# Performance work log

Measured on AMD Instinct MI355X. Metric: run time of the kernel, lower is better.

The kernel has to match this reference:

```python
import jax, jax.numpy as jnp
import numpy as np

B, N, M = 4, 2048, 2048
DIM, DIM_KEYS, DIM_OUT = 512, 512, 512
HEADS, DIM_HEAD = 8, 64
INNER = HEADS * DIM_HEAD


def setup_inputs() -> dict:
    key = jax.random.key(0)
    ks = jax.random.split(key, 8)
    x = jax.random.normal(ks[0], (B, N, DIM), dtype=jnp.float32)
    context = jax.random.normal(ks[1], (B, M, DIM_KEYS), dtype=jnp.float32)
    Wq = jax.random.normal(ks[2], (DIM, INNER), dtype=jnp.float32) / np.sqrt(DIM)
    Wkv = jax.random.normal(ks[3], (DIM_KEYS, 2 * INNER), dtype=jnp.float32) / np.sqrt(DIM_KEYS)
    null_k = jax.random.normal(ks[4], (DIM_HEAD,), dtype=jnp.float32)
    null_v = jax.random.normal(ks[5], (DIM_HEAD,), dtype=jnp.float32)
    Wout = jax.random.normal(ks[6], (INNER, DIM_OUT), dtype=jnp.float32) / np.sqrt(INNER)
    bout = jnp.zeros((DIM_OUT,), dtype=jnp.float32)
    return {"x": x, "context": context, "Wq": Wq, "Wkv": Wkv,
            "null_k": null_k, "null_v": null_v, "Wout": Wout, "bout": bout}


def reference(x, context, Wq, Wkv, null_k, null_v, Wout, bout):
    b = x.shape[0]
    scale = DIM_HEAD ** (-0.5)
    q = x @ Wq                      # [b, n, inner]
    kv = context @ Wkv              # [b, m, 2*inner]
    k, v = jnp.split(kv, 2, axis=-1)
    # [b, h, n, d]
    q = q.reshape(b, -1, HEADS, DIM_HEAD).transpose(0, 2, 1, 3)
    k = k.reshape(b, -1, HEADS, DIM_HEAD).transpose(0, 2, 1, 3)
    v = v.reshape(b, -1, HEADS, DIM_HEAD).transpose(0, 2, 1, 3)
    # prepend null key/value token: [b, h, 1, d]
    nk = jnp.broadcast_to(null_k, (b, HEADS, 1, DIM_HEAD))
    nv = jnp.broadcast_to(null_v, (b, HEADS, 1, DIM_HEAD))
    k = jnp.concatenate((nk, k), axis=-2)  # [b, h, m+1, d]
    v = jnp.concatenate((nv, v), axis=-2)
    q = jnp.tanh(q)
    k = jnp.tanh(k)
    sim = jnp.einsum('bhid,bhjd->bhij', q, k) * scale  # [b, h, n, m+1]
    attn = jax.nn.softmax(sim, axis=-1)
    out = jnp.einsum('bhij,bhjd->bhid', attn, v)       # [b, h, n, d]
    out = out.transpose(0, 2, 1, 3).reshape(b, -1, INNER)  # [b, n, inner]
    return out @ Wout + bout
```

## Files before the change

### kernel.cpp

```cpp
#include <hip/hip_runtime.h>
#include <hip/hip_bf16.h>
#include <stdint.h>

#define B_    4
#define N_    2048
#define M_    2048
#define DIMX  512
#define INNER 512
#define H_    8
#define DH    64
#define MK    2049
#define MKP   2112

#define QSCALE  0.18033688011f
#define SM_BIAS -11.5415605f

using u16 = unsigned short;
using u32 = unsigned int;

typedef __attribute__((ext_vector_type(8))) short short8;
typedef __attribute__((ext_vector_type(4))) float f32x4;

#if defined(__has_builtin)
# if __has_builtin(__builtin_amdgcn_exp2f)
#  define EXP2(x) __builtin_amdgcn_exp2f(x)
# endif
#endif
#ifndef EXP2
# define EXP2(x) exp2f(x)
#endif

__device__ __forceinline__ u16 bfc(float f){
  __hip_bfloat16 h = __float2bfloat16(f);
  return *reinterpret_cast<u16*>(&h);
}
__device__ __forceinline__ u32 bfpk(float lo, float hi){
  return (u32)bfc(lo) | ((u32)bfc(hi) << 16);
}

__global__ __launch_bounds__(256) void transpose_all(
    const float* __restrict__ Wq, const float* __restrict__ Wkv,
    const float* __restrict__ Wout,
    u16* __restrict__ Wqt, u16* __restrict__ Wkvt, u16* __restrict__ Woutt)
{
  const int z = blockIdx.z;
  const float* in = (z == 0) ? Wq : (z == 1) ? Wkv : Wout;
  u16* out        = (z == 0) ? Wqt : (z == 1) ? Wkvt : Woutt;
  const int C     = (z == 1) ? 1024 : 512;
  const int R     = 512;
  if (blockIdx.x * 64 >= C) return;

  __shared__ float tl[64][65];
  const int t = threadIdx.x;
  const int c0 = blockIdx.x * 64, r0 = blockIdx.y * 64;
  const int col = t & 63, rb = t >> 6;
  #pragma unroll
  for (int j = 0; j < 16; ++j){
    const int row = rb + j*4;
    tl[row][col] = in[(size_t)(r0 + row) * C + c0 + col];
  }
  __syncthreads();
  #pragma unroll
  for (int j = 0; j < 16; ++j){
    const int orow = rb + j*4;
    out[(size_t)(c0 + orow) * R + r0 + col] = bfc(tl[col][orow]);
  }
}

__global__ __launch_bounds__(256, 3) void fused_proj(
    const float* __restrict__ x, const float* __restrict__ ctx,
    const u16* __restrict__ Wqt, const u16* __restrict__ Wkvt,
    u16* __restrict__ qb, u16* __restrict__ kb, u16* __restrict__ vb)
{
  __shared__ __align__(16) short At[2][128*32];
  __shared__ __align__(16) short Bl[2][128*32];

  const int flat = blockIdx.x;
  const int tile = (flat & 7) * 96 + (flat >> 3);
  const bool isq = tile < 256;
  const int lt   = isq ? tile : tile - 256;
  const int gx   = isq ? 4 : 8;
  const int row0 = (lt / gx) * 128, col0 = (lt % gx) * 128;
  const float* A = isq ? x : ctx;
  const u16*  Bt = isq ? Wqt : Wkvt;

  const int tid = threadIdx.x;
  const int w = tid >> 6, lane = tid & 63;
  const int c = lane & 15, g = lane >> 4;
  const int wr = (w >> 1) * 64, wc = (w & 1) * 64;

  f32x4 acc[4][4] = {};

  const int srow = tid >> 1, sj = (tid & 1) * 2;
  const int swz0 = ((sj  ) ^ ((srow >> 1) & 3)) << 4;
  const int swz1 = ((sj+1) ^ ((srow >> 1) & 3)) << 4;

  float4 a0, a1, a2, a3;
  uint4  b0, b1;
  const float* asrc = A  + (size_t)(row0 + srow) * DIMX + sj*8;
  const u16*   bsrc = Bt + (size_t)(col0 + srow) * DIMX + sj*8;

  a0 = ((const float4*)asrc)[0]; a1 = ((const float4*)asrc)[1];
  a2 = ((const float4*)asrc)[2]; a3 = ((const float4*)asrc)[3];
  b0 = ((const uint4*)bsrc)[0];  b1 = ((const uint4*)bsrc)[1];
  {
    uint4 t0, t1;
    t0.x = bfpk(a0.x, a0.y); t0.y = bfpk(a0.z, a0.w);
    t0.z = bfpk(a1.x, a1.y); t0.w = bfpk(a1.z, a1.w);
    t1.x = bfpk(a2.x, a2.y); t1.y = bfpk(a2.z, a2.w);
    t1.z = bfpk(a3.x, a3.y); t1.w = bfpk(a3.z, a3.w);
    *(uint4*)((char*)At[0] + srow*64 + swz0) = t0;
    *(uint4*)((char*)At[0] + srow*64 + swz1) = t1;
    *(uint4*)((char*)Bl[0] + srow*64 + swz0) = b0;
    *(uint4*)((char*)Bl[0] + srow*64 + swz1) = b1;
  }

  int cur = 0;
  #pragma unroll 4
  for (int kk = 0; kk < 16; ++kk){
    __syncthreads();
    if (kk < 15){
      const float* an = asrc + (kk+1)*32;
      const u16*   bn = bsrc + (kk+1)*32;
      a0 = ((const float4*)an)[0]; a1 = ((const float4*)an)[1];
      a2 = ((const float4*)an)[2]; a3 = ((const float4*)an)[3];
      b0 = ((const uint4*)bn)[0];  b1 = ((const uint4*)bn)[1];
    }

    short8 af[4], bf[4];
    #pragma unroll
    for (int m = 0; m < 4; ++m){
      const int row = wr + m*16 + c;
      af[m] = *(const short8*)((char*)At[cur] + row*64 + ((g ^ ((row>>1)&3)) << 4));
    }
    #pragma unroll
    for (int n = 0; n < 4; ++n){
      const int row = wc + n*16 + c;
      bf[n] = *(const short8*)((char*)Bl[cur] + row*64 + ((g ^ ((row>>1)&3)) << 4));
    }
    __builtin_amdgcn_s_setprio(1);
    #pragma unroll
    for (int m = 0; m < 4; ++m)
      #pragma unroll
      for (int n = 0; n < 4; ++n)
        acc[m][n] = __builtin_amdgcn_mfma_f32_16x16x32_bf16(af[m], bf[n], acc[m][n], 0, 0, 0);
    __builtin_amdgcn_s_setprio(0);

    if (kk < 15){
      uint4 t0, t1;
      t0.x = bfpk(a0.x, a0.y); t0.y = bfpk(a0.z, a0.w);
      t0.z = bfpk(a1.x, a1.y); t0.w = bfpk(a1.z, a1.w);
      t1.x = bfpk(a2.x, a2.y); t1.y = bfpk(a2.z, a2.w);
      t1.z = bfpk(a3.x, a3.y); t1.w = bfpk(a3.z, a3.w);
      char* An = (char*)At[cur ^ 1];
      char* Bn = (char*)Bl[cur ^ 1];
      *(uint4*)(An + srow*64 + swz0) = t0;
      *(uint4*)(An + srow*64 + swz1) = t1;
      *(uint4*)(Bn + srow*64 + swz0) = b0;
      *(uint4*)(Bn + srow*64 + swz1) = b1;
      cur ^= 1;
    }
  }

  #pragma unroll
  for (int m = 0; m < 4; ++m){
    #pragma unroll
    for (int n = 0; n < 4; ++n){
      #pragma unroll
      for (int rr = 0; rr < 4; ++rr){
        const int R = row0 + wr + m*16 + g*4 + rr;
        const int col = col0 + wc + n*16 + c;
        const float v = acc[m][n][rr];
        if (isq){
          qb[(size_t)R * INNER + col] = bfc(tanhf(v) * QSCALE);
        } else {
          const int bidx = R >> 11, mm = R & 2047;
          if (col < INNER){
            const int h = col >> 6, d = col & 63;
            kb[((size_t)(bidx*H_ + h) * MKP + (mm + 1)) * DH + d] = bfc(tanhf(v));
          } else {
            const int cc = col - INNER;
            const int h = cc >> 6, d = cc & 63;
            vb[((size_t)(bidx*H_ + h) * MKP + (mm + 1)) * DH + d] = bfc(v);
          }
        }
      }
    }
  }
}

__global__ __launch_bounds__(256) void mgemm_out(
    const u16* __restrict__ A, const u16* __restrict__ Bt,
    float* __restrict__ Cf, const float* __restrict__ bias)
{
  __shared__ __align__(16) short At[2][128*32];
  __shared__ __align__(16) short Bl[2][128*32];

  const int flat = blockIdx.x;
  const int tile = (flat & 7) * 32 + (flat >> 3);
  const int row0 = (tile >> 2) * 128, col0 = (tile & 3) * 128;

  const int tid = threadIdx.x;
  const int w = tid >> 6, lane = tid & 63;
  const int c = lane & 15, g = lane >> 4;
  const int wr = (w >> 1) * 64, wc = (w & 1) * 64;

  f32x4 acc[4][4] = {};

  const int srow = tid >> 1, sj = (tid & 1) * 2;
  const int swz0 = ((sj  ) ^ ((srow >> 1) & 3)) << 4;
  const int swz1 = ((sj+1) ^ ((srow >> 1) & 3)) << 4;

  uint4 ta0, ta1, b0, b1;
  const u16* asrc = A  + (size_t)(row0 + srow) * INNER + sj*8;
  const u16* bsrc = Bt + (size_t)(col0 + srow) * INNER + sj*8;

  ta0 = ((const uint4*)asrc)[0]; ta1 = ((const uint4*)asrc)[1];
  b0  = ((const uint4*)bsrc)[0]; b1  = ((const uint4*)bsrc)[1];
  *(uint4*)((char*)At[0] + srow*64 + swz0) = ta0;
  *(uint4*)((char*)At[0] + srow*64 + swz1) = ta1;
  *(uint4*)((char*)Bl[0] + srow*64 + swz0) = b0;
  *(uint4*)((char*)Bl[0] + srow*64 + swz1) = b1;

  int cur = 0;
  #pragma unroll 4
  for (int kk = 0; kk < 16; ++kk){
    __syncthreads();
    if (kk < 15){
      const u16* an = asrc + (kk+1)*32;
      const u16* bn = bsrc + (kk+1)*32;
      ta0 = ((const uint4*)an)[0]; ta1 = ((const uint4*)an)[1];
      b0  = ((const uint4*)bn)[0]; b1  = ((const uint4*)bn)[1];
    }

    short8 af[4], bf[4];
    #pragma unroll
    for (int m = 0; m < 4; ++m){
      const int row = wr + m*16 + c;
      af[m] = *(const short8*)((char*)At[cur] + row*64 + ((g ^ ((row>>1)&3)) << 4));
    }
    #pragma unroll
    for (int n = 0; n < 4; ++n){
      const int row = wc + n*16 + c;
      bf[n] = *(const short8*)((char*)Bl[cur] + row*64 + ((g ^ ((row>>1)&3)) << 4));
    }
    __builtin_amdgcn_s_setprio(1);
    #pragma unroll
    for (int m = 0; m < 4; ++m)
      #pragma unroll
      for (int n = 0; n < 4; ++n)
        acc[m][n] = __builtin_amdgcn_mfma_f32_16x16x32_bf16(af[m], bf[n], acc[m][n], 0, 0, 0);
    __builtin_amdgcn_s_setprio(0);

    if (kk < 15){
      char* An = (char*)At[cur ^ 1];
      char* Bn = (char*)Bl[cur ^ 1];
      *(uint4*)(An + srow*64 + swz0) = ta0;
      *(uint4*)(An + srow*64 + swz1) = ta1;
      *(uint4*)(Bn + srow*64 + swz0) = b0;
      *(uint4*)(Bn + srow*64 + swz1) = b1;
      cur ^= 1;
    }
  }

  #pragma unroll
  for (int m = 0; m < 4; ++m){
    #pragma unroll
    for (int n = 0; n < 4; ++n){
      #pragma unroll
      for (int rr = 0; rr < 4; ++rr){
        const int R = row0 + wr + m*16 + g*4 + rr;
        const int col = col0 + wc + n*16 + c;
        Cf[(size_t)R * 512 + col] = acc[m][n][rr] + bias[col];
      }
    }
  }
}

__global__ __launch_bounds__(256) void vtrans(
    const u16* __restrict__ vb, u16* __restrict__ vt,
    const float* __restrict__ nk, const float* __restrict__ nv,
    u16* __restrict__ kb)
{
  __shared__ short tl[64][72];
  const int t = threadIdx.x;
  const int mt = blockIdx.x, bh = blockIdx.y;
  {
    const int mr = t >> 2, chb = (t & 3) * 2;
    const u16* src = vb + ((size_t)bh * MKP + mt*64 + mr) * DH + chb*8;
    uint4 a = ((const uint4*)src)[0];
    uint4 b = ((const uint4*)src)[1];
    *(uint4*)((char*)tl + mr*144 + chb*16)     = a;
    *(uint4*)((char*)tl + mr*144 + (chb+1)*16) = b;
  }
  __syncthreads();
  {
    const int d = t >> 2, chb = (t & 3) * 2;
    #pragma unroll
    for (int j = 0; j < 2; ++j){
      const int mbase = (chb + j) * 8;
      u16 s[8];
      #pragma unroll
      for (int e = 0; e < 8; ++e) s[e] = (u16)tl[mbase + e][d];
      if (mt == 0 && mbase == 0) s[0] = bfc(nv[d]);
      uint4 o;
      o.x = (u32)s[0] | ((u32)s[1] << 16);
      o.y = (u32)s[2] | ((u32)s[3] << 16);
      o.z = (u32)s[4] | ((u32)s[5] << 16);
      o.w = (u32)s[6] | ((u32)s[7] << 16);
      *(uint4*)(vt + ((size_t)bh * DH + d) * MKP + mt*64 + mbase) = o;
    }
    if (mt == 0 && (t & 3) == 0)
      kb[(size_t)bh * MKP * DH + d] = bfc(tanhf(nk[d]));
  }
}

__global__ __launch_bounds__(256) void attn_mfma(
    const u16* __restrict__ qb, const u16* __restrict__ kb,
    const u16* __restrict__ vt, u16* __restrict__ aob)
{
  __shared__ __align__(16) short Kl[2][64*64];
  __shared__ __align__(16) short Vl[2][64*64];
  __shared__ __align__(16) short Pl[4][16*64];

  const int tid  = threadIdx.x;
  const int w    = tid >> 6;
  const int lane = tid & 63;
  const int c    = lane & 15;
  const int g    = lane >> 4;
  const int bh   = blockIdx.y, b = bh >> 3, h = bh & 7;
  const int qbase = blockIdx.x * 64 + w * 16;
  const int xr   = (c & 7) << 4;

  short8 qf0, qf1;
  {
    const u16* qrow = qb + ((size_t)(b*N_) + qbase + c) * INNER + h * DH;
    qf0 = *(const short8*)(qrow + g*8);
    qf1 = *(const short8*)(qrow + 32 + g*8);
  }

  f32x4 o[4] = {};
  float l_c = 0.f;

  const u16* kbase = kb + (size_t)bh * MKP * DH;
  const u16* vbase = vt + (size_t)bh * DH * MKP;
  const int srow = tid >> 2, sch = (tid & 3) * 2;
  const int swz0 = ((sch  ) ^ (srow & 7)) << 4;
  const int swz1 = ((sch+1) ^ (srow & 7)) << 4;

  uint4 rk0, rk1, rv0, rv1;
  {
    const u16* ksrc = kbase + (size_t)srow * DH + sch*8;
    rk0 = ((const uint4*)ksrc)[0]; rk1 = ((const uint4*)ksrc)[1];
    const u16* vsrc = vbase + (size_t)srow * MKP + sch*8;
    rv0 = ((const uint4*)vsrc)[0]; rv1 = ((const uint4*)vsrc)[1];
  }
  *(uint4*)((char*)Kl[0] + srow*128 + swz0) = rk0;
  *(uint4*)((char*)Kl[0] + srow*128 + swz1) = rk1;
  *(uint4*)((char*)Vl[0] + srow*128 + swz0) = rv0;
  *(uint4*)((char*)Vl[0] + srow*128 + swz1) = rv1;

  int cur = 0;
  for (int kt = 0; kt < 33; ++kt){
    __syncthreads();
    if (kt < 32){
      const u16* ksrc = kbase + (size_t)((kt+1)*64 + srow) * DH + sch*8;
      rk0 = ((const uint4*)ksrc)[0]; rk1 = ((const uint4*)ksrc)[1];
      const u16* vsrc = vbase + (size_t)srow * MKP + (kt+1)*64 + sch*8;
      rv0 = ((const uint4*)vsrc)[0]; rv1 = ((const uint4*)vsrc)[1];
    }

    const char* Kc = (const char*)Kl[cur];
    const char* Vc = (const char*)Vl[cur];
    char*       Pw = (char*)Pl + w*2048;

    f32x4 sv[4];
    __builtin_amdgcn_s_setprio(1);
    #pragma unroll
    for (int s = 0; s < 4; ++s){
      f32x4 a = {SM_BIAS, SM_BIAS, SM_BIAS, SM_BIAS};
      #pragma unroll
      for (int hh = 0; hh < 2; ++hh){
        short8 kf = *(const short8*)(Kc + (s*16 + c)*128 + ((hh*64 + g*16) ^ xr));
        a = __builtin_amdgcn_mfma_f32_16x16x32_bf16(kf, hh ? qf1 : qf0, a, 0, 0, 0);
      }
      sv[s] = a;
    }
    __builtin_amdgcn_s_setprio(0);

    if (kt == 32){
      #pragma unroll
      for (int s = 0; s < 4; ++s)
        #pragma unroll
        for (int r = 0; r < 4; ++r)
          if (s | r) sv[s][r] = -1e30f;
      if (g) sv[0][0] = -1e30f;
    }

    float psum = 0.f;
    #pragma unroll
    for (int s = 0; s < 4; ++s){
      const float p0 = EXP2(sv[s][0]);
      const float p1 = EXP2(sv[s][1]);
      const float p2 = EXP2(sv[s][2]);
      const float p3 = EXP2(sv[s][3]);
      psum += (p0 + p1) + (p2 + p3);
      uint2 pk;
      pk.x = bfpk(p0, p1);
      pk.y = bfpk(p2, p3);
      *(uint2*)(Pw + c*128 + ((((2*s + (g>>1)) ^ (c&7)) << 4) | ((g&1)*8))) = pk;
    }
    psum += __shfl_xor(psum, 16);
    psum += __shfl_xor(psum, 32);
    l_c += psum;

    __builtin_amdgcn_s_setprio(1);
    #pragma unroll
    for (int hh = 0; hh < 2; ++hh){
      short8 pf = *(const short8*)(Pw + c*128 + (((hh*4 + g) ^ (c&7)) << 4));
      #pragma unroll
      for (int D = 0; D < 4; ++D){
        short8 vf = *(const short8*)(Vc + (D*16 + c)*128 + ((hh*64 + g*16) ^ xr));
        o[D] = __builtin_amdgcn_mfma_f32_16x16x32_bf16(pf, vf, o[D], 0, 0, 0);
      }
    }
    __builtin_amdgcn_s_setprio(0);

    if (kt < 32){
      char* Kn = (char*)Kl[cur ^ 1];
      char* Vn = (char*)Vl[cur ^ 1];
      *(uint4*)(Kn + srow*128 + swz0) = rk0;
      *(uint4*)(Kn + srow*128 + swz1) = rk1;
      *(uint4*)(Vn + srow*128 + swz0) = rv0;
      *(uint4*)(Vn + srow*128 + swz1) = rv1;
      cur ^= 1;
    }
  }

  const float inv = 1.f / l_c;
  #pragma unroll
  for (int r = 0; r < 4; ++r){
    const float ir = __shfl(inv, g*4 + r, 16);
    const size_t nrow = (size_t)(b*N_) + qbase + g*4 + r;
    #pragma unroll
    for (int D = 0; D < 4; ++D)
      aob[nrow * INNER + h*DH + D*16 + c] = bfc(o[D][r] * ir);
  }
}

extern "C" void kernel_launch(void* const* d_in, const int* in_sizes, int n_in,
                              void* d_out, int out_size, void* d_ws, size_t ws_size,
                              hipStream_t stream)
{
  const float* x    = (const float*)d_in[0];
  const float* ctx  = (const float*)d_in[1];
  const float* Wq   = (const float*)d_in[2];
  const float* Wkv  = (const float*)d_in[3];
  const float* nk   = (const float*)d_in[4];
  const float* nv   = (const float*)d_in[5];
  const float* Wout = (const float*)d_in[6];
  const float* bout = (const float*)d_in[7];
  float* out = (float*)d_out;

  char* ws = (char*)d_ws;
  u16* qb    = (u16*)(ws);
  u16* kbB   = (u16*)(ws +  8388608);
  u16* vbB   = (u16*)(ws + 17039360);
  u16* vtb   = (u16*)(ws + 25690112);
  u16* Wqt   = (u16*)(ws + 34340864);
  u16* Wkvt  = (u16*)(ws + 34865152);
  u16* Woutt = (u16*)(ws + 35913728);
  u16* aoB   = vbB;

  transpose_all<<<dim3(16, 8, 3), 256, 0, stream>>>(Wq, Wkv, Wout, Wqt, Wkvt, Woutt);

  fused_proj<<<768, 256, 0, stream>>>(x, ctx, Wqt, Wkvt, qb, kbB, vbB);
  vtrans<<<dim3(33, 32), 256, 0, stream>>>(vbB, vtb, nk, nv, kbB);
  attn_mfma<<<dim3(32, 32), 256, 0, stream>>>(qb, kbB, vtb, aoB);
  mgemm_out<<<256, 256, 0, stream>>>(aoB, Woutt, out, bout);
}
```

Baseline: 121.9 us.

## Pre-convert inputs to bf16, deepen GEMM prefetch, remap attention grid

Adds a separate kernel that converts x and context to bf16 ahead of time, so the projection GEMM loads bf16 directly instead of converting fp32 inside its main loop. Both GEMMs now keep two k-tiles of global loads in flight, using a manually unrolled double-register prefetch. mgemm_out gets an occupancy hint in its launch bounds. The attention launch becomes a 1D grid with the block index remapped so that head/batch pairs are spread across XCDs. The cost is an extra kernel launch and an extra fp32 read and bf16 write/read of the activations.

```diff
diff --git a/kernel.cpp b/kernel.cpp
--- a/kernel.cpp
+++ b/kernel.cpp
@@ -38,6 +38,21 @@
   return (u32)bfc(lo) | ((u32)bfc(hi) << 16);
 }
 
+__global__ __launch_bounds__(256) void convert_bf(
+    const float* __restrict__ x, const float* __restrict__ ctx,
+    u16* __restrict__ xb, u16* __restrict__ cb)
+{
+  const float* in = blockIdx.z ? ctx : x;
+  u16* out        = blockIdx.z ? cb : xb;
+  const int i = blockIdx.x * 256 + threadIdx.x;
+  float4 a = ((const float4*)in)[i*2];
+  float4 b = ((const float4*)in)[i*2+1];
+  uint4 t;
+  t.x = bfpk(a.x, a.y); t.y = bfpk(a.z, a.w);
+  t.z = bfpk(b.x, b.y); t.w = bfpk(b.z, b.w);
+  ((uint4*)out)[i] = t;
+}
+
 __global__ __launch_bounds__(256) void transpose_all(
     const float* __restrict__ Wq, const float* __restrict__ Wkv,
     const float* __restrict__ Wout,
@@ -67,8 +82,30 @@
   }
 }
 
+#define PROJ_COMPUTE(bi)                                                      \
+  {                                                                           \
+    short8 af[4], bf[4];                                                      \
+    _Pragma("unroll")                                                         \
+    for (int m = 0; m < 4; ++m){                                              \
+      const int row = wr + m*16 + c;                                          \
+      af[m] = *(const short8*)((char*)At[bi] + row*64 + ((g ^ ((row>>1)&3)) << 4)); \
+    }                                                                         \
+    _Pragma("unroll")                                                         \
+    for (int n = 0; n < 4; ++n){                                              \
+      const int row = wc + n*16 + c;                                          \
+      bf[n] = *(const short8*)((char*)Bl[bi] + row*64 + ((g ^ ((row>>1)&3)) << 4)); \
+    }                                                                         \
+    __builtin_amdgcn_s_setprio(1);                                            \
+    _Pragma("unroll")                                                         \
+    for (int m = 0; m < 4; ++m)                                               \
+      _Pragma("unroll")                                                       \
+      for (int n = 0; n < 4; ++n)                                             \
+        acc[m][n] = __builtin_amdgcn_mfma_f32_16x16x32_bf16(af[m], bf[n], acc[m][n], 0, 0, 0); \
+    __builtin_amdgcn_s_setprio(0);                                            \
+  }
+
 __global__ __launch_bounds__(256, 3) void fused_proj(
-    const float* __restrict__ x, const float* __restrict__ ctx,
+    const u16* __restrict__ xb, const u16* __restrict__ cb,
     const u16* __restrict__ Wqt, const u16* __restrict__ Wkvt,
     u16* __restrict__ qb, u16* __restrict__ kb, u16* __restrict__ vb)
 {
@@ -81,8 +118,8 @@
   const int lt   = isq ? tile : tile - 256;
   const int gx   = isq ? 4 : 8;
   const int row0 = (lt / gx) * 128, col0 = (lt % gx) * 128;
-  const float* A = isq ? x : ctx;
-  const u16*  Bt = isq ? Wqt : Wkvt;
+  const u16* A  = isq ? xb : cb;
+  const u16* Bt = isq ? Wqt : Wkvt;
 
   const int tid = threadIdx.x;
   const int w = tid >> 6, lane = tid & 63;
@@ -95,70 +132,48 @@
   const int swz0 = ((sj  ) ^ ((srow >> 1) & 3)) << 4;
   const int swz1 = ((sj+1) ^ ((srow >> 1) & 3)) << 4;
 
-  float4 a0, a1, a2, a3;
-  uint4  b0, b1;
-  const float* asrc = A  + (size_t)(row0 + srow) * DIMX + sj*8;
-  const u16*   bsrc = Bt + (size_t)(col0 + srow) * DIMX + sj*8;
-
-  a0 = ((const float4*)asrc)[0]; a1 = ((const float4*)asrc)[1];
-  a2 = ((const float4*)asrc)[2]; a3 = ((const float4*)asrc)[3];
-  b0 = ((const uint4*)bsrc)[0];  b1 = ((const uint4*)bsrc)[1];
-  {
-    uint4 t0, t1;
-    t0.x = bfpk(a0.x, a0.y); t0.y = bfpk(a0.z, a0.w);
-    t0.z = bfpk(a1.x, a1.y); t0.w = bfpk(a1.z, a1.w);
-    t1.x = bfpk(a2.x, a2.y); t1.y = bfpk(a2.z, a2.w);
-    t1.z = bfpk(a3.x, a3.y); t1.w = bfpk(a3.z, a3.w);
-    *(uint4*)((char*)At[0] + srow*64 + swz0) = t0;
-    *(uint4*)((char*)At[0] + srow*64 + swz1) = t1;
-    *(uint4*)((char*)Bl[0] + srow*64 + swz0) = b0;
-    *(uint4*)((char*)Bl[0] + srow*64 + swz1) = b1;
-  }
-
-  int cur = 0;
-  #pragma unroll 4
-  for (int kk = 0; kk < 16; ++kk){
+  const u16* asrc = A  + (size_t)(row0 + srow) * DIMX + sj*8;
+  const u16* bsrc = Bt + (size_t)(col0 + srow) * DIMX + sj*8;
+
+  uint4 aA0, aA1, bA0, bA1;
+  uint4 aB0, aB1, bB0, bB1;
+
+  aA0 = ((const uint4*)asrc)[0];        aA1 = ((const uint4*)asrc)[1];
+  bA0 = ((const uint4*)bsrc)[0];        bA1 = ((const uint4*)bsrc)[1];
+  aB0 = ((const uint4*)(asrc + 32))[0]; aB1 = ((const uint4*)(asrc + 32))[1];
+  bB0 = ((const uint4*)(bsrc + 32))[0]; bB1 = ((const uint4*)(bsrc + 32))[1];
+  *(uint4*)((char*)At[0] + srow*64 + swz0) = aA0;
+  *(uint4*)((char*)At[0] + srow*64 + swz1) = aA1;
+  *(uint4*)((char*)Bl[0] + srow*64 + swz0) = bA0;
+  *(uint4*)((char*)Bl[0] + srow*64 + swz1) = bA1;
+
+  for (int kk = 0; kk < 16; kk += 2){
     __syncthreads();
-    if (kk < 15){
-      const float* an = asrc + (kk+1)*32;
-      const u16*   bn = bsrc + (kk+1)*32;
-      a0 = ((const float4*)an)[0]; a1 = ((const float4*)an)[1];
-      a2 = ((const float4*)an)[2]; a3 = ((const float4*)an)[3];
-      b0 = ((const uint4*)bn)[0];  b1 = ((const uint4*)bn)[1];
-    }
-
-    short8 af[4], bf[4];
-    #pragma unroll
-    for (int m = 0; m < 4; ++m){
-      const int row = wr + m*16 + c;
-      af[m] = *(const short8*)((char*)At[cur] + row*64 + ((g ^ ((row>>1)&3)) << 4));
-    }
-    #pragma unroll
-    for (int n = 0; n < 4; ++n){
-      const int row = wc + n*16 + c;
-      bf[n] = *(const short8*)((char*)Bl[cur] + row*64 + ((g ^ ((row>>1)&3)) << 4));
-    }
-    __builtin_amdgcn_s_setprio(1);
-    #pragma unroll
-    for (int m = 0; m < 4; ++m)
-      #pragma unroll
-      for (int n = 0; n < 4; ++n)
-        acc[m][n] = __builtin_amdgcn_mfma_f32_16x16x32_bf16(af[m], bf[n], acc[m][n], 0, 0, 0);
-    __builtin_amdgcn_s_setprio(0);
-
-    if (kk < 15){
-      uint4 t0, t1;
-      t0.x = bfpk(a0.x, a0.y); t0.y = bfpk(a0.z, a0.w);
-      t0.z = bfpk(a1.x, a1.y); t0.w = bfpk(a1.z, a1.w);
-      t1.x = bfpk(a2.x, a2.y); t1.y = bfpk(a2.z, a2.w);
-      t1.z = bfpk(a3.x, a3.y); t1.w = bfpk(a3.z, a3.w);
-      char* An = (char*)At[cur ^ 1];
-      char* Bn = (char*)Bl[cur ^ 1];
-      *(uint4*)(An + srow*64 + swz0) = t0;
-      *(uint4*)(An + srow*64 + swz1) = t1;
-      *(uint4*)(Bn + srow*64 + swz0) = b0;
-      *(uint4*)(Bn + srow*64 + swz1) = b1;
-      cur ^= 1;
+    if (kk + 2 < 16){
+      const u16* an = asrc + (kk+2)*32;
+      const u16* bn = bsrc + (kk+2)*32;
+      aA0 = ((const uint4*)an)[0]; aA1 = ((const uint4*)an)[1];
+      bA0 = ((const uint4*)bn)[0]; bA1 = ((const uint4*)bn)[1];
+    }
+    PROJ_COMPUTE(0);
+    *(uint4*)((char*)At[1] + srow*64 + swz0) = aB0;
+    *(uint4*)((char*)At[1] + srow*64 + swz1) = aB1;
+    *(uint4*)((char*)Bl[1] + srow*64 + swz0) = bB0;
+    *(uint4*)((char*)Bl[1] + srow*64 + swz1) = bB1;
+
+    __syncthreads();
+    if (kk + 3 < 16){
+      const u16* an = asrc + (kk+3)*32;
+      const u16* bn = bsrc + (kk+3)*32;
+      aB0 = ((const uint4*)an)[0]; aB1 = ((const uint4*)an)[1];
+      bB0 = ((const uint4*)bn)[0]; bB1 = ((const uint4*)bn)[1];
+    }
+    PROJ_COMPUTE(1);
+    if (kk + 2 < 16){
+      *(uint4*)((char*)At[0] + srow*64 + swz0) = aA0;
+      *(uint4*)((char*)At[0] + srow*64 + swz1) = aA1;
+      *(uint4*)((char*)Bl[0] + srow*64 + swz0) = bA0;
+      *(uint4*)((char*)Bl[0] + srow*64 + swz1) = bA1;
     }
   }
 
@@ -189,7 +204,7 @@
   }
 }
 
-__global__ __launch_bounds__(256) void mgemm_out(
+__global__ __launch_bounds__(256, 3) void mgemm_out(
     const u16* __restrict__ A, const u16* __restrict__ Bt,
     float* __restrict__ Cf, const float* __restrict__ bias)
 {
@@ -211,55 +226,48 @@
   const int swz0 = ((sj  ) ^ ((srow >> 1) & 3)) << 4;
   const int swz1 = ((sj+1) ^ ((srow >> 1) & 3)) << 4;
 
-  uint4 ta0, ta1, b0, b1;
   const u16* asrc = A  + (size_t)(row0 + srow) * INNER + sj*8;
   const u16* bsrc = Bt + (size_t)(col0 + srow) * INNER + sj*8;
 
-  ta0 = ((const uint4*)asrc)[0]; ta1 = ((const uint4*)asrc)[1];
-  b0  = ((const uint4*)bsrc)[0]; b1  = ((const uint4*)bsrc)[1];
-  *(uint4*)((char*)At[0] + srow*64 + swz0) = ta0;
-  *(uint4*)((char*)At[0] + srow*64 + swz1) = ta1;
-  *(uint4*)((char*)Bl[0] + srow*64 + swz0) = b0;
-  *(uint4*)((char*)Bl[0] + srow*64 + swz1) = b1;
-
-  int cur = 0;
-  #pragma unroll 4
-  for (int kk = 0; kk < 16; ++kk){
+  uint4 aA0, aA1, bA0, bA1;
+  uint4 aB0, aB1, bB0, bB1;
+
+  aA0 = ((const uint4*)asrc)[0];        aA1 = ((const uint4*)asrc)[1];
+  bA0 = ((const uint4*)bsrc)[0];        bA1 = ((const uint4*)bsrc)[1];
+  aB0 = ((const uint4*)(asrc + 32))[0]; aB1 = ((const uint4*)(asrc + 32))[1];
+  bB0 = ((const uint4*)(bsrc + 32))[0]; bB1 = ((const uint4*)(bsrc + 32))[1];
+  *(uint4*)((char*)At[0] + srow*64 + swz0) = aA0;
+  *(uint4*)((char*)At[0] + srow*64 + swz1) = aA1;
+  *(uint4*)((char*)Bl[0] + srow*64 + swz0) = bA0;
+  *(uint4*)((char*)Bl[0] + srow*64 + swz1) = bA1;
+
+  for (int kk = 0; kk < 16; kk += 2){
     __syncthreads();
-    if (kk < 15){
-      const u16* an = asrc + (kk+1)*32;
-      const u16* bn = bsrc + (kk+1)*32;
-      ta0 = ((const uint4*)an)[0]; ta1 = ((const uint4*)an)[1];
-      b0  = ((const uint4*)bn)[0]; b1  = ((const uint4*)bn)[1];
-    }
-
-    short8 af[4], bf[4];
-    #pragma unroll
-    for (int m = 0; m < 4; ++m){
-      const int row = wr + m*16 + c;
-      af[m] = *(const short8*)((char*)At[cur] + row*64 + ((g ^ ((row>>1)&3)) << 4));
-    }
-    #pragma unroll
-    for (int n = 0; n < 4; ++n){
-      const int row = wc + n*16 + c;
-      bf[n] = *(const short8*)((char*)Bl[cur] + row*64 + ((g ^ ((row>>1)&3)) << 4));
-    }
-    __builtin_amdgcn_s_setprio(1);
-    #pragma unroll
-    for (int m = 0; m < 4; ++m)
-      #pragma unroll
-      for (int n = 0; n < 4; ++n)
-        acc[m][n] = __builtin_amdgcn_mfma_f32_16x16x32_bf16(af[m], bf[n], acc[m][n], 0, 0, 0);
-    __builtin_amdgcn_s_setprio(0);
-
-    if (kk < 15){
-      char* An = (char*)At[cur ^ 1];
-      char* Bn = (char*)Bl[cur ^ 1];
-      *(uint4*)(An + srow*64 + swz0) = ta0;
-      *(uint4*)(An + srow*64 + swz1) = ta1;
-      *(uint4*)(Bn + srow*64 + swz0) = b0;
-      *(uint4*)(Bn + srow*64 + swz1) = b1;
-      cur ^= 1;
+    if (kk + 2 < 16){
+      const u16* an = asrc + (kk+2)*32;
+      const u16* bn = bsrc + (kk+2)*32;
+      aA0 = ((const uint4*)an)[0]; aA1 = ((const uint4*)an)[1];
+      bA0 = ((const uint4*)bn)[0]; bA1 = ((const uint4*)bn)[1];
+    }
+    PROJ_COMPUTE(0);
+    *(uint4*)((char*)At[1] + srow*64 + swz0) = aB0;
+    *(uint4*)((char*)At[1] + srow*64 + swz1) = aB1;
+    *(uint4*)((char*)Bl[1] + srow*64 + swz0) = bB0;
+    *(uint4*)((char*)Bl[1] + srow*64 + swz1) = bB1;
+
+    __syncthreads();
+    if (kk + 3 < 16){
+      const u16* an = asrc + (kk+3)*32;
+      const u16* bn = bsrc + (kk+3)*32;
+      aB0 = ((const uint4*)an)[0]; aB1 = ((const uint4*)an)[1];
+      bB0 = ((const uint4*)bn)[0]; bB1 = ((const uint4*)bn)[1];
+    }
+    PROJ_COMPUTE(1);
+    if (kk + 2 < 16){
+      *(uint4*)((char*)At[0] + srow*64 + swz0) = aA0;
+      *(uint4*)((char*)At[0] + srow*64 + swz1) = aA1;
+      *(uint4*)((char*)Bl[0] + srow*64 + swz0) = bA0;
+      *(uint4*)((char*)Bl[0] + srow*64 + swz1) = bA1;
     }
   }
 
@@ -328,8 +336,11 @@
   const int lane = tid & 63;
   const int c    = lane & 15;
   const int g    = lane >> 4;
-  const int bh   = blockIdx.y, b = bh >> 3, h = bh & 7;
-  const int qbase = blockIdx.x * 64 + w * 16;
+  const int L    = blockIdx.x;
+  const int cc   = L >> 3;
+  const int bh   = (L & 7) * 4 + (cc >> 5);
+  const int b    = bh >> 3, h = bh & 7;
+  const int qbase = (cc & 31) * 64 + w * 16;
   const int xr   = (c & 7) << 4;
 
   short8 qf0, qf1;
@@ -463,19 +474,22 @@
   float* out = (float*)d_out;
 
   char* ws = (char*)d_ws;
-  u16* qb    = (u16*)(ws);
-  u16* kbB   = (u16*)(ws +  8388608);
-  u16* vbB   = (u16*)(ws + 17039360);
-  u16* vtb   = (u16*)(ws + 25690112);
-  u16* Wqt   = (u16*)(ws + 34340864);
-  u16* Wkvt  = (u16*)(ws + 34865152);
-  u16* Woutt = (u16*)(ws + 35913728);
+  u16* xb    = (u16*)(ws);
+  u16* cb    = (u16*)(ws +  8388608);
+  u16* qb    = (u16*)(ws + 16777216);
+  u16* kbB   = (u16*)(ws + 25165824);
+  u16* vbB   = (u16*)(ws + 33816576);
+  u16* vtb   = (u16*)(ws + 42467328);
+  u16* Wqt   = (u16*)(ws + 51118080);
+  u16* Wkvt  = (u16*)(ws + 51642368);
+  u16* Woutt = (u16*)(ws + 52690944);
   u16* aoB   = vbB;
 
+  convert_bf<<<dim3(2048, 1, 2), 256, 0, stream>>>(x, ctx, xb, cb);
   transpose_all<<<dim3(16, 8, 3), 256, 0, stream>>>(Wq, Wkv, Wout, Wqt, Wkvt, Woutt);
 
-  fused_proj<<<768, 256, 0, stream>>>(x, ctx, Wqt, Wkvt, qb, kbB, vbB);
+  fused_proj<<<768, 256, 0, stream>>>(xb, cb, Wqt, Wkvt, qb, kbB, vbB);
   vtrans<<<dim3(33, 32), 256, 0, stream>>>(vbB, vtb, nk, nv, kbB);
-  attn_mfma<<<dim3(32, 32), 256, 0, stream>>>(qb, kbB, vtb, aoB);
+  attn_mfma<<<1024, 256, 0, stream>>>(qb, kbB, vtb, aoB);
   mgemm_out<<<256, 256, 0, stream>>>(aoB, Woutt, out, bout);
 }
```

New measurement: 118.6 us. 2.7% less time.
